# Kernel optimization log

Hardware: AMD Instinct MI355X
Metric: run time of the kernel (lower is better)

Reference implementation:

```python
import jax, jax.numpy as jnp
import numpy as np

B, T, D, H = 4, 2048, 1024, 16
HD = D // H  # head_dim = 64

def setup_inputs() -> dict:
    key = jax.random.key(0)
    k1, k2, k3 = jax.random.split(key, 3)
    s = 1.0 / np.sqrt(D)
    x = jax.random.normal(k1, (B, T, D), dtype=jnp.float32)
    W_qkv = jax.random.normal(k2, (D, 3 * D), dtype=jnp.float32) * s
    W_proj = jax.random.normal(k3, (D, D), dtype=jnp.float32) * s
    return {"x": x, "W_qkv": W_qkv, "W_proj": W_proj}

def reference(x, W_qkv, W_proj):
    Bq, Tq, C = x.shape
    qkv = x @ W_qkv                                   # [B,T,3C]
    q, k, v = jnp.split(qkv, 3, axis=-1)
    def heads(t):  # [B,T,C] -> [B,H,T,HD]
        return t.reshape(Bq, Tq, H, HD).transpose(0, 2, 1, 3)
    q, k, v = heads(q), heads(k), heads(v)
    scale = 1.0 / np.sqrt(HD)
    att = jnp.einsum('bhqd,bhkd->bhqk', q, k) * scale  # [B,H,T,T]
    causal = jnp.tril(jnp.ones((Tq, Tq), dtype=bool))
    att = jnp.where(causal[None, None], att, -jnp.inf)
    att = jax.nn.softmax(att, axis=-1)
    y = jnp.einsum('bhqk,bhkd->bhqd', att, v)          # [B,H,T,HD]
    y = y.transpose(0, 2, 1, 3).reshape(Bq, Tq, C)
    return y @ W_proj
```

## Files before the change

kernel.cpp:

```cpp
#include <hip/hip_runtime.h>

typedef unsigned short ushort_t;
typedef __attribute__((ext_vector_type(8))) __bf16 bf16x8;
typedef __attribute__((ext_vector_type(4))) float f32x4;
typedef __attribute__((ext_vector_type(16))) float f32x16;
typedef __attribute__((ext_vector_type(4))) float float4v;
typedef __attribute__((ext_vector_type(8))) unsigned short ushort8v;
typedef __attribute__((ext_vector_type(4))) unsigned short ushort4v;
typedef __attribute__((ext_vector_type(4))) unsigned uint4v;

#define T_LEN 2048
#define D_DIM 1024
#define NHEAD 16
#define HDIM 64
#define BH 64
#define MROWS 8192
#define PERQKV ((size_t)BH * T_LEN * HDIM)

__device__ __forceinline__ ushort_t f2bf(float f) {
  unsigned u = __builtin_bit_cast(unsigned, f);
  u = (u + 0x7FFFu + ((u >> 16) & 1u)) >> 16;
  return (ushort_t)u;
}

__device__ __forceinline__ float fast_exp2(float x) {
  float r; asm("v_exp_f32 %0, %1" : "=v"(r) : "v"(x)); return r;
}

__device__ __forceinline__ void load_lds16(const ushort_t* g, ushort_t* l) {
  __builtin_amdgcn_global_load_lds((const __attribute__((address_space(1))) void*)g,
                                   (__attribute__((address_space(3))) void*)l, 16, 0, 0);
}

__global__ __launch_bounds__(256) void k_cvt_x(const float* __restrict__ x,
                                               ushort_t* __restrict__ xb) {
  int i = blockIdx.x * 256 + threadIdx.x;
  float4v v = ((const float4v*)x)[i];
  ushort4v o;
  o[0] = f2bf(v[0]); o[1] = f2bf(v[1]); o[2] = f2bf(v[2]); o[3] = f2bf(v[3]);
  ((ushort4v*)xb)[i] = o;
}

__global__ __launch_bounds__(256) void k_transpose(const float* __restrict__ W,
                                                   ushort_t* __restrict__ Wt,
                                                   int R, int C) {
  __shared__ ushort_t tile[32][33];
  int tx = threadIdx.x & 31, ty = threadIdx.x >> 5;
  int r0 = blockIdx.y << 5, c0 = blockIdx.x << 5;
#pragma unroll
  for (int i = 0; i < 4; ++i) {
    int r = ty + i * 8;
    tile[r][tx] = f2bf(W[(size_t)(r0 + r) * C + c0 + tx]);
  }
  __syncthreads();
#pragma unroll
  for (int i = 0; i < 4; ++i) {
    int r = ty + i * 8;
    Wt[(size_t)(c0 + r) * R + r0 + tx] = tile[tx][r];
  }
}

template <int N, int K, int EPI>
__global__ __launch_bounds__(256) void k_gemm(const ushort_t* __restrict__ A,
                                              const ushort_t* __restrict__ Bt,
                                              ushort_t* __restrict__ O16,
                                              float* __restrict__ O32) {
  __shared__ __align__(16) ushort_t Atile[128 * 32];
  __shared__ __align__(16) ushort_t Btile[128 * 32];
  const int tid = threadIdx.x;
  const int lane = tid & 63, w = tid >> 6;
  const int g = lane >> 4, c = lane & 15;
  const int wm = w >> 1, wn = w & 1;
  const int m0 = blockIdx.y * 128, n0 = blockIdx.x * 128;

  f32x4 acc[4][4];
#pragma unroll
  for (int i = 0; i < 4; ++i)
#pragma unroll
    for (int j = 0; j < 4; ++j) acc[i][j] = (f32x4){0.f, 0.f, 0.f, 0.f};

  for (int k0 = 0; k0 < K; k0 += 32) {
    __syncthreads();
#pragma unroll
    for (int r = 0; r < 2; ++r) {
      int flat = r * 256 + tid;
      int row = flat >> 2, slot = flat & 3;
      int gsl = slot ^ (row & 3);
      load_lds16(A + (size_t)(m0 + row) * K + k0 + gsl * 8,
                 &Atile[(r * 256 + w * 64) * 8]);
      load_lds16(Bt + (size_t)(n0 + row) * K + k0 + gsl * 8,
                 &Btile[(r * 256 + w * 64) * 8]);
    }
    __syncthreads();

    bf16x8 af[4], bfr[4];
#pragma unroll
    for (int mi = 0; mi < 4; ++mi) {
      int row = wm * 64 + mi * 16 + c;
      int sl = g ^ (row & 3);
      af[mi] = *(const bf16x8*)&Atile[row * 32 + sl * 8];
    }
#pragma unroll
    for (int ni = 0; ni < 4; ++ni) {
      int row = wn * 64 + ni * 16 + c;
      int sl = g ^ (row & 3);
      bfr[ni] = *(const bf16x8*)&Btile[row * 32 + sl * 8];
    }
#pragma unroll
    for (int mi = 0; mi < 4; ++mi)
#pragma unroll
      for (int ni = 0; ni < 4; ++ni)
        acc[mi][ni] = __builtin_amdgcn_mfma_f32_16x16x32_bf16(af[mi], bfr[ni],
                                                              acc[mi][ni], 0, 0, 0);
  }

#pragma unroll
  for (int mi = 0; mi < 4; ++mi)
#pragma unroll
    for (int ni = 0; ni < 4; ++ni) {
      int n = n0 + wn * 64 + ni * 16 + c;
#pragma unroll
      for (int j = 0; j < 4; ++j) {
        int m = m0 + wm * 64 + mi * 16 + g * 4 + j;
        float v = acc[mi][ni][j];
        if constexpr (EPI == 0) {
          int which = n >> 10, hn = n & 1023;
          int h = hn >> 6, d = hn & 63;
          int b = m >> 11, t = m & 2047;
          if (which == 0) v *= 0.18033688f;
          O16[(size_t)which * PERQKV +
              (((size_t)(b * NHEAD + h) * T_LEN + t) * HDIM + d)] = f2bf(v);
        } else {
          O32[(size_t)m * N + n] = v;
        }
      }
    }
}

template <int NB_TILES, int EPI>
__global__ __launch_bounds__(512, 2) void k_gemm3(const ushort_t* __restrict__ A,
                                                  const ushort_t* __restrict__ Bt,
                                                  ushort_t* __restrict__ O16,
                                                  float* __restrict__ O32) {
  __shared__ __align__(16) ushort_t As[3][128 * 64];
  __shared__ __align__(16) ushort_t Bs[3][256 * 64];
  const int tid = threadIdx.x, lane = tid & 63, w = tid >> 6;
  const int g = lane >> 4, c = lane & 15;
  const int wm = w & 1, wn = w >> 1;
  const int nblk = 64 * NB_TILES;
  const int chunk = nblk >> 3;
  const int bid = blockIdx.x;
  const int logical = (bid & 7) * chunk + (bid >> 3);
  const int mb = logical & 63, nb = logical >> 6;
  const int m0 = mb * 128, n0 = nb * 256;

  const int srow = lane >> 3, sgran = lane & 7;

  auto stage = [&](int t, int buf) {
    const int k0 = t * 64;
#pragma unroll
    for (int l = 0; l < 2; ++l) {
      int r = w * 16 + l * 8 + srow;
      load_lds16(A + (size_t)(m0 + r) * 1024 + k0 + ((sgran ^ (r & 7)) << 3),
                 &As[buf][(w * 16 + l * 8) * 64]);
    }
#pragma unroll
    for (int l = 0; l < 4; ++l) {
      int r = w * 32 + l * 8 + srow;
      load_lds16(Bt + (size_t)(n0 + r) * 1024 + k0 + ((sgran ^ (r & 7)) << 3),
                 &Bs[buf][(w * 32 + l * 8) * 64]);
    }
  };

  f32x4 acc[4][4];
#pragma unroll
  for (int i = 0; i < 4; ++i)
#pragma unroll
    for (int j = 0; j < 4; ++j) acc[i][j] = (f32x4){0.f, 0.f, 0.f, 0.f};

  stage(0, 0);
  stage(1, 1);

  for (int t = 0; t < 16; ++t) {
    if (t < 15) asm volatile("s_waitcnt vmcnt(6)" ::: "memory");
    else        asm volatile("s_waitcnt vmcnt(0)" ::: "memory");
    __builtin_amdgcn_s_barrier();
    __builtin_amdgcn_sched_barrier(0);

    if (t + 2 < 16) stage(t + 2, (t + 2) % 3);

    const int cur = t % 3;
    const ushort_t* abuf = &As[cur][0];
    const ushort_t* bbuf = &Bs[cur][0];
#pragma unroll
    for (int kk = 0; kk < 2; ++kk) {
      bf16x8 af[4], bq[4];
#pragma unroll
      for (int fr = 0; fr < 4; ++fr) {
        int r = wm * 64 + fr * 16 + c;
        af[fr] = *(const bf16x8*)&abuf[r * 64 + (((kk * 4 + g) ^ (r & 7)) << 3)];
      }
#pragma unroll
      for (int fc = 0; fc < 4; ++fc) {
        int r = wn * 64 + fc * 16 + c;
        bq[fc] = *(const bf16x8*)&bbuf[r * 64 + (((kk * 4 + g) ^ (r & 7)) << 3)];
      }
      __builtin_amdgcn_s_setprio(1);
#pragma unroll
      for (int fr = 0; fr < 4; ++fr)
#pragma unroll
        for (int fc = 0; fc < 4; ++fc)
          acc[fr][fc] = __builtin_amdgcn_mfma_f32_16x16x32_bf16(af[fr], bq[fc],
                                                                acc[fr][fc], 0, 0, 0);
      __builtin_amdgcn_s_setprio(0);
    }
  }

#pragma unroll
  for (int fr = 0; fr < 4; ++fr)
#pragma unroll
    for (int fc = 0; fc < 4; ++fc) {
      int n = n0 + wn * 64 + fc * 16 + c;
#pragma unroll
      for (int j = 0; j < 4; ++j) {
        int m = m0 + wm * 64 + fr * 16 + g * 4 + j;
        float v = acc[fr][fc][j];
        if constexpr (EPI == 0) {
          int which = n >> 10, hn = n & 1023;
          int h = hn >> 6, d = hn & 63;
          int b = m >> 11, tt = m & 2047;
          if (which == 0) v *= 0.18033688f;
          O16[(size_t)which * PERQKV +
              (((size_t)(b * NHEAD + h) * T_LEN + tt) * HDIM + d)] = f2bf(v);
        } else {
          O32[(size_t)m * (64 * NB_TILES * 4) + n] = v;
        }
      }
    }
}

__global__ __launch_bounds__(128, 4) void k_attn(const ushort_t* __restrict__ Q,
                                                 const ushort_t* __restrict__ Kv,
                                                 const ushort_t* __restrict__ Vv,
                                                 ushort_t* __restrict__ Y) {
  __shared__ __align__(16) ushort_t Kt[2][64 * 64];
  __shared__ __align__(16) ushort_t Vt[2][64 * 64];

  const int bid = blockIdx.x;
  const int bh = (bid & 7) * 8 + ((bid >> 3) & 7);
  const int pairidx = bid >> 6;
  const int pA = 31 - pairidx, pB = pairidx;
  const int nktA = pA + 1;
  const int total = nktA + pB + 1;

  const int tid = threadIdx.x, lane = tid & 63, w = tid >> 6;
  const int hi = lane >> 5, lc = lane & 31;
  const size_t base = (size_t)bh * (T_LEN * HDIM);

  int q32 = pA * 64 + w * 32;
  bf16x8 qf[4];
#pragma unroll
  for (int st = 0; st < 4; ++st)
    qf[st] = *(const bf16x8*)(Q + base + (size_t)(q32 + lc) * HDIM + st * 16 + hi * 8);

  f32x16 o0, o1;
#pragma unroll
  for (int i = 0; i < 16; ++i) { o0[i] = 0.f; o1[i] = 0.f; }
  float mrun = 0.f, lrun = 0.f;

  const int ksl = tid & 7, krow0 = tid >> 3;
  const int kpair = tid & 31, vk0 = 2 * kpair, vd0 = (tid >> 5) * 8;

  bf16x8 kreg[4];
  ushort8v vreg[4];
  auto stage_issue = [&](int kt) {
    const ushort_t* kb = Kv + base + (size_t)kt * 64 * HDIM;
    const ushort_t* vb = Vv + base + (size_t)kt * 64 * HDIM;
    vreg[0] = *(const ushort8v*)(vb + (size_t)vk0 * HDIM + vd0);
    vreg[1] = *(const ushort8v*)(vb + (size_t)(vk0 + 1) * HDIM + vd0);
    vreg[2] = *(const ushort8v*)(vb + (size_t)vk0 * HDIM + vd0 + 32);
    vreg[3] = *(const ushort8v*)(vb + (size_t)(vk0 + 1) * HDIM + vd0 + 32);
#pragma unroll
    for (int m = 0; m < 4; ++m)
      kreg[m] = *(const bf16x8*)(kb + (size_t)(krow0 + 16 * m) * HDIM + ksl * 8);
  };
  auto stage_write = [&](int buf) {
#pragma unroll
    for (int m = 0; m < 4; ++m) {
      int r = krow0 + 16 * m;
      *(bf16x8*)&Kt[buf][r * 64 + ((ksl ^ (r & 7)) << 3)] = kreg[m];
    }
#pragma unroll
    for (int e = 0; e < 8; ++e) {
      int rd = vd0 + e;
      unsigned pv = (unsigned)vreg[0][e] | ((unsigned)vreg[1][e] << 16);
      *(unsigned*)&Vt[buf][rd * 64 + (((kpair >> 2) ^ (rd & 7)) << 3) + 2 * (kpair & 3)] = pv;
      int rd2 = rd + 32;
      unsigned pv2 = (unsigned)vreg[2][e] | ((unsigned)vreg[3][e] << 16);
      *(unsigned*)&Vt[buf][rd2 * 64 + (((kpair >> 2) ^ (rd2 & 7)) << 3) + 2 * (kpair & 3)] = pv2;
    }
  };

  const int b_ = bh >> 4, h_ = bh & 15;
  auto epilogue = [&]() {
    float lt = lrun + __shfl_xor(lrun, 32);
    float invl = 1.f / lt;
#pragma unroll
    for (int r = 0; r < 16; ++r) {
      int cr = (r & 3) + 8 * (r >> 2) + 4 * hi;
      float iv = __shfl(invl, cr);
      size_t m = (size_t)b_ * T_LEN + q32 + cr;
      Y[m * D_DIM + h_ * HDIM + lc]      = f2bf(o0[r] * iv);
      Y[m * D_DIM + h_ * HDIM + 32 + lc] = f2bf(o1[r] * iv);
    }
  };

  stage_issue(0); stage_write(0);
  stage_issue(1);
  __syncthreads();

  for (int it = 0; it < total; ++it) {
    if (it == nktA) {
      epilogue();
      q32 = pB * 64 + w * 32;
#pragma unroll
      for (int st = 0; st < 4; ++st)
        qf[st] = *(const bf16x8*)(Q + base + (size_t)(q32 + lc) * HDIM + st * 16 + hi * 8);
#pragma unroll
      for (int i = 0; i < 16; ++i) { o0[i] = 0.f; o1[i] = 0.f; }
      mrun = 0.f; lrun = 0.f;
    }
    const int kt = (it < nktA) ? it : it - nktA;
    const int cur = it & 1;
    const ushort_t* kbuf = &Kt[cur][0];
    const ushort_t* vbuf = &Vt[cur][0];

    f32x16 s0, s1;
#pragma unroll
    for (int i = 0; i < 16; ++i) { s0[i] = 0.f; s1[i] = 0.f; }
    __builtin_amdgcn_s_setprio(1);
#pragma unroll
    for (int st = 0; st < 4; ++st) {
      bf16x8 kf0 = *(const bf16x8*)&kbuf[lc * 64 + (((2 * st + hi) ^ (lc & 7)) << 3)];
      s0 = __builtin_amdgcn_mfma_f32_32x32x16_bf16(kf0, qf[st], s0, 0, 0, 0);
    }
#pragma unroll
    for (int st = 0; st < 4; ++st) {
      bf16x8 kf1 = *(const bf16x8*)&kbuf[(32 + lc) * 64 + (((2 * st + hi) ^ (lc & 7)) << 3)];
      s1 = __builtin_amdgcn_mfma_f32_32x32x16_bf16(kf1, qf[st], s1, 0, 0, 0);
    }
    __builtin_amdgcn_s_setprio(0);

    if (kt * 64 + 63 > q32) {
      const int q = q32 + lc;
#pragma unroll
      for (int r = 0; r < 16; ++r) {
        int cr = (r & 3) + 8 * (r >> 2) + 4 * hi;
        if (kt * 64 + cr > q)      s0[r] = -3.0e38f;
        if (kt * 64 + 32 + cr > q) s1[r] = -3.0e38f;
      }
    }

    float tm[8];
#pragma unroll
    for (int i = 0; i < 8; ++i) tm[i] = fmaxf(fmaxf(s0[i], s0[i + 8]), fmaxf(s1[i], s1[i + 8]));
#pragma unroll
    for (int i = 0; i < 4; ++i) tm[i] = fmaxf(tm[i], tm[i + 4]);
    float tmax = fmaxf(fmaxf(tm[0], tm[1]), fmaxf(tm[2], tm[3]));
    tmax = fmaxf(tmax, __shfl_xor(tmax, 32));

    if (!__all(tmax <= mrun + 11.0f)) {
      float mnew = fmaxf(mrun, tmax);
      float sc = fast_exp2(mrun - mnew);
      lrun *= sc; mrun = mnew;
#pragma unroll
      for (int r = 0; r < 16; ++r) {
        int cr = (r & 3) + 8 * (r >> 2) + 4 * hi;
        float scr = __shfl(sc, cr);
        o0[r] *= scr; o1[r] *= scr;
      }
    }

#pragma unroll
    for (int r = 0; r < 16; ++r) s0[r] = fast_exp2(s0[r] - mrun);
#pragma unroll
    for (int r = 0; r < 16; ++r) s1[r] = fast_exp2(s1[r] - mrun);
    {
      float u0 = 0.f, u1 = 0.f, u2 = 0.f, u3 = 0.f;
#pragma unroll
      for (int i = 0; i < 4; ++i) {
        u0 += s0[i];     u1 += s0[i + 4];  u2 += s0[i + 8];  u3 += s0[i + 12];
        u0 += s1[i];     u1 += s1[i + 4];  u2 += s1[i + 8];  u3 += s1[i + 12];
      }
      lrun += (u0 + u1) + (u2 + u3);
    }

    unsigned wv[16];
#pragma unroll
    for (int i = 0; i < 8; ++i) {
      asm("v_cvt_pk_bf16_f32 %0, %1, %2" : "=v"(wv[i])     : "v"(s0[2 * i]), "v"(s0[2 * i + 1]));
      asm("v_cvt_pk_bf16_f32 %0, %1, %2" : "=v"(wv[8 + i]) : "v"(s1[2 * i]), "v"(s1[2 * i + 1]));
    }
    bf16x8 pf[4];
#pragma unroll
    for (int g4 = 0; g4 < 4; ++g4) {
      unsigned a0 = wv[4 * g4], a1 = wv[4 * g4 + 1];
      unsigned a2 = wv[4 * g4 + 2], a3 = wv[4 * g4 + 3];
      asm("v_permlane32_swap_b32 %0, %1" : "+v"(a0), "+v"(a2));
      asm("v_permlane32_swap_b32 %0, %1" : "+v"(a1), "+v"(a3));
      uint4v fw; fw[0] = a0; fw[1] = a1; fw[2] = a2; fw[3] = a3;
      pf[g4] = __builtin_bit_cast(bf16x8, fw);
    }

    __builtin_amdgcn_s_setprio(1);
#pragma unroll
    for (int km = 0; km < 4; ++km) {
      int gsl = ((2 * km + hi) ^ (lc & 7)) << 3;
      bf16x8 vb0 = *(const bf16x8*)&vbuf[lc * 64 + gsl];
      bf16x8 vb1 = *(const bf16x8*)&vbuf[(32 + lc) * 64 + gsl];
      o0 = __builtin_amdgcn_mfma_f32_32x32x16_bf16(pf[km], vb0, o0, 0, 0, 0);
      o1 = __builtin_amdgcn_mfma_f32_32x32x16_bf16(pf[km], vb1, o1, 0, 0, 0);
    }
    __builtin_amdgcn_s_setprio(0);

    if (it + 1 < total) stage_write((it + 1) & 1);
    if (it + 2 < total) {
      int itn = it + 2;
      stage_issue((itn < nktA) ? itn : itn - nktA);
    }
    __syncthreads();
  }

  epilogue();
}

extern "C" void kernel_launch(void* const* d_in, const int* in_sizes, int n_in,
                              void* d_out, int out_size, void* d_ws, size_t ws_size,
                              hipStream_t stream) {
  const float* x     = (const float*)d_in[0];
  const float* Wqkv  = (const float*)d_in[1];
  const float* Wproj = (const float*)d_in[2];
  float* out = (float*)d_out;
  ushort_t* ws = (ushort_t*)d_ws;

  ushort_t* Xb  = ws;
  ushort_t* WqT = Xb  + (size_t)MROWS * D_DIM;
  ushort_t* WpT = WqT + (size_t)3 * D_DIM * D_DIM;
  ushort_t* Qb  = WpT + (size_t)D_DIM * D_DIM;
  ushort_t* Kb  = Qb + PERQKV;
  ushort_t* Vb  = Kb + PERQKV;
  ushort_t* Yb  = Vb + PERQKV;

  k_cvt_x<<<(MROWS * D_DIM / 4) / 256, 256, 0, stream>>>(x, Xb);
  k_transpose<<<dim3(3 * D_DIM / 32, D_DIM / 32), 256, 0, stream>>>(Wqkv, WqT, D_DIM, 3 * D_DIM);
  k_transpose<<<dim3(D_DIM / 32, D_DIM / 32), 256, 0, stream>>>(Wproj, WpT, D_DIM, D_DIM);
  k_gemm<3 * D_DIM, D_DIM, 0><<<dim3(3 * D_DIM / 128, MROWS / 128), 256, 0, stream>>>(Xb, WqT, Qb, nullptr);
  k_attn<<<1024, 128, 0, stream>>>(Qb, Kb, Vb, Yb);
  k_gemm3<4, 1><<<256, 512, 0, stream>>>(Yb, WpT, nullptr, out);
}
```

Baseline: 186.0 us.

## Merge prep kernels, compute softmax denominator via MFMA, use v_perm V staging

New measurement: 175.3 us. 5.8% less time.

```diff
diff --git a/kernel.cpp b/kernel.cpp
--- a/kernel.cpp
+++ b/kernel.cpp
@@ -26,27 +26,39 @@
 __device__ __forceinline__ float fast_exp2(float x) {
   float r; asm("v_exp_f32 %0, %1" : "=v"(r) : "v"(x)); return r;
 }
+__device__ __forceinline__ float fast_rcp(float x) {
+  float r; asm("v_rcp_f32 %0, %1" : "=v"(r) : "v"(x)); return r;
+}
 
 __device__ __forceinline__ void load_lds16(const ushort_t* g, ushort_t* l) {
   __builtin_amdgcn_global_load_lds((const __attribute__((address_space(1))) void*)g,
                                    (__attribute__((address_space(3))) void*)l, 16, 0, 0);
 }
 
-__global__ __launch_bounds__(256) void k_cvt_x(const float* __restrict__ x,
-                                               ushort_t* __restrict__ xb) {
-  int i = blockIdx.x * 256 + threadIdx.x;
-  float4v v = ((const float4v*)x)[i];
-  ushort4v o;
-  o[0] = f2bf(v[0]); o[1] = f2bf(v[1]); o[2] = f2bf(v[2]); o[3] = f2bf(v[3]);
-  ((ushort4v*)xb)[i] = o;
-}
-
-__global__ __launch_bounds__(256) void k_transpose(const float* __restrict__ W,
-                                                   ushort_t* __restrict__ Wt,
-                                                   int R, int C) {
+__global__ __launch_bounds__(256) void k_prep(const float* __restrict__ x,
+                                              const float* __restrict__ Wqkv,
+                                              const float* __restrict__ Wproj,
+                                              ushort_t* __restrict__ xb,
+                                              ushort_t* __restrict__ WqT,
+                                              ushort_t* __restrict__ WpT) {
   __shared__ ushort_t tile[32][33];
-  int tx = threadIdx.x & 31, ty = threadIdx.x >> 5;
-  int r0 = blockIdx.y << 5, c0 = blockIdx.x << 5;
+  int bid = blockIdx.x, tid = threadIdx.x;
+  if (bid < 8192) {
+    int i = bid * 256 + tid;
+    float4v v = ((const float4v*)x)[i];
+    ushort4v o;
+    o[0] = f2bf(v[0]); o[1] = f2bf(v[1]); o[2] = f2bf(v[2]); o[3] = f2bf(v[3]);
+    ((ushort4v*)xb)[i] = o;
+    return;
+  }
+  bid -= 8192;
+  int bx = bid & 127, by = bid >> 7;
+  const float* W; ushort_t* Wt; int C;
+  if (bx < 96) { W = Wqkv; Wt = WqT; C = 3072; }
+  else         { W = Wproj; Wt = WpT; C = 1024; bx -= 96; }
+  const int R = 1024;
+  int tx = tid & 31, ty = tid >> 5;
+  int r0 = by << 5, c0 = bx << 5;
 #pragma unroll
   for (int i = 0; i < 4; ++i) {
     int r = ty + i * 8;
@@ -239,7 +251,7 @@
     }
 }
 
-__global__ __launch_bounds__(128, 4) void k_attn(const ushort_t* __restrict__ Q,
+__global__ __launch_bounds__(128, 2) void k_attn(const ushort_t* __restrict__ Q,
                                                  const ushort_t* __restrict__ Kv,
                                                  const ushort_t* __restrict__ Vv,
                                                  ushort_t* __restrict__ Y) {
@@ -257,16 +269,22 @@
   const int hi = lane >> 5, lc = lane & 31;
   const size_t base = (size_t)bh * (T_LEN * HDIM);
 
+  f32x16 z16;
+#pragma unroll
+  for (int i = 0; i < 16; ++i) z16[i] = 0.f;
+  uint4v ow; ow[0] = ow[1] = ow[2] = ow[3] = 0x3F803F80u;
+  const bf16x8 onesf = __builtin_bit_cast(bf16x8, ow);
+
   int q32 = pA * 64 + w * 32;
   bf16x8 qf[4];
 #pragma unroll
   for (int st = 0; st < 4; ++st)
     qf[st] = *(const bf16x8*)(Q + base + (size_t)(q32 + lc) * HDIM + st * 16 + hi * 8);
 
-  f32x16 o0, o1;
-#pragma unroll
-  for (int i = 0; i < 16; ++i) { o0[i] = 0.f; o1[i] = 0.f; }
-  float mrun = 0.f, lrun = 0.f;
+  f32x16 o0, o1, ol;
+#pragma unroll
+  for (int i = 0; i < 16; ++i) { o0[i] = 0.f; o1[i] = 0.f; ol[i] = 0.f; }
+  float mrun = 0.f;
 
   const int ksl = tid & 7, krow0 = tid >> 3;
   const int kpair = tid & 31, vk0 = 2 * kpair, vd0 = (tid >> 5) * 8;
@@ -290,25 +308,34 @@
       int r = krow0 + 16 * m;
       *(bf16x8*)&Kt[buf][r * 64 + ((ksl ^ (r & 7)) << 3)] = kreg[m];
     }
-#pragma unroll
-    for (int e = 0; e < 8; ++e) {
-      int rd = vd0 + e;
-      unsigned pv = (unsigned)vreg[0][e] | ((unsigned)vreg[1][e] << 16);
-      *(unsigned*)&Vt[buf][rd * 64 + (((kpair >> 2) ^ (rd & 7)) << 3) + 2 * (kpair & 3)] = pv;
+    uint4v a0 = __builtin_bit_cast(uint4v, vreg[0]);
+    uint4v a1 = __builtin_bit_cast(uint4v, vreg[1]);
+    uint4v a2 = __builtin_bit_cast(uint4v, vreg[2]);
+    uint4v a3 = __builtin_bit_cast(uint4v, vreg[3]);
+#pragma unroll
+    for (int i = 0; i < 4; ++i) {
+      unsigned lo, hi2, lo2, hi3;
+      asm("v_perm_b32 %0, %1, %2, %3" : "=v"(lo)  : "v"(a1[i]), "v"(a0[i]), "s"(0x05040100u));
+      asm("v_perm_b32 %0, %1, %2, %3" : "=v"(hi2) : "v"(a1[i]), "v"(a0[i]), "s"(0x07060302u));
+      asm("v_perm_b32 %0, %1, %2, %3" : "=v"(lo2) : "v"(a3[i]), "v"(a2[i]), "s"(0x05040100u));
+      asm("v_perm_b32 %0, %1, %2, %3" : "=v"(hi3) : "v"(a3[i]), "v"(a2[i]), "s"(0x07060302u));
+      int rd = vd0 + 2 * i;
+      *(unsigned*)&Vt[buf][rd * 64 + (((kpair >> 2) ^ (rd & 7)) << 3) + 2 * (kpair & 3)] = lo;
+      int rd1 = rd + 1;
+      *(unsigned*)&Vt[buf][rd1 * 64 + (((kpair >> 2) ^ (rd1 & 7)) << 3) + 2 * (kpair & 3)] = hi2;
       int rd2 = rd + 32;
-      unsigned pv2 = (unsigned)vreg[2][e] | ((unsigned)vreg[3][e] << 16);
-      *(unsigned*)&Vt[buf][rd2 * 64 + (((kpair >> 2) ^ (rd2 & 7)) << 3) + 2 * (kpair & 3)] = pv2;
+      *(unsigned*)&Vt[buf][rd2 * 64 + (((kpair >> 2) ^ (rd2 & 7)) << 3) + 2 * (kpair & 3)] = lo2;
+      int rd3 = rd + 33;
+      *(unsigned*)&Vt[buf][rd3 * 64 + (((kpair >> 2) ^ (rd3 & 7)) << 3) + 2 * (kpair & 3)] = hi3;
     }
   };
 
   const int b_ = bh >> 4, h_ = bh & 15;
   auto epilogue = [&]() {
-    float lt = lrun + __shfl_xor(lrun, 32);
-    float invl = 1.f / lt;
 #pragma unroll
     for (int r = 0; r < 16; ++r) {
       int cr = (r & 3) + 8 * (r >> 2) + 4 * hi;
-      float iv = __shfl(invl, cr);
+      float iv = fast_rcp(ol[r]);
       size_t m = (size_t)b_ * T_LEN + q32 + cr;
       Y[m * D_DIM + h_ * HDIM + lc]      = f2bf(o0[r] * iv);
       Y[m * D_DIM + h_ * HDIM + 32 + lc] = f2bf(o1[r] * iv);
@@ -327,27 +354,28 @@
       for (int st = 0; st < 4; ++st)
         qf[st] = *(const bf16x8*)(Q + base + (size_t)(q32 + lc) * HDIM + st * 16 + hi * 8);
 #pragma unroll
-      for (int i = 0; i < 16; ++i) { o0[i] = 0.f; o1[i] = 0.f; }
-      mrun = 0.f; lrun = 0.f;
+      for (int i = 0; i < 16; ++i) { o0[i] = 0.f; o1[i] = 0.f; ol[i] = 0.f; }
+      mrun = 0.f;
     }
     const int kt = (it < nktA) ? it : it - nktA;
     const int cur = it & 1;
     const ushort_t* kbuf = &Kt[cur][0];
     const ushort_t* vbuf = &Vt[cur][0];
 
-    f32x16 s0, s1;
-#pragma unroll
-    for (int i = 0; i < 16; ++i) { s0[i] = 0.f; s1[i] = 0.f; }
     __builtin_amdgcn_s_setprio(1);
-#pragma unroll
-    for (int st = 0; st < 4; ++st) {
-      bf16x8 kf0 = *(const bf16x8*)&kbuf[lc * 64 + (((2 * st + hi) ^ (lc & 7)) << 3)];
-      s0 = __builtin_amdgcn_mfma_f32_32x32x16_bf16(kf0, qf[st], s0, 0, 0, 0);
-    }
-#pragma unroll
-    for (int st = 0; st < 4; ++st) {
-      bf16x8 kf1 = *(const bf16x8*)&kbuf[(32 + lc) * 64 + (((2 * st + hi) ^ (lc & 7)) << 3)];
-      s1 = __builtin_amdgcn_mfma_f32_32x32x16_bf16(kf1, qf[st], s1, 0, 0, 0);
+    bf16x8 kf0 = *(const bf16x8*)&kbuf[lc * 64 + ((hi ^ (lc & 7)) << 3)];
+    f32x16 s0 = __builtin_amdgcn_mfma_f32_32x32x16_bf16(kf0, qf[0], z16, 0, 0, 0);
+#pragma unroll
+    for (int st = 1; st < 4; ++st) {
+      bf16x8 kf = *(const bf16x8*)&kbuf[lc * 64 + (((2 * st + hi) ^ (lc & 7)) << 3)];
+      s0 = __builtin_amdgcn_mfma_f32_32x32x16_bf16(kf, qf[st], s0, 0, 0, 0);
+    }
+    bf16x8 kg0 = *(const bf16x8*)&kbuf[(32 + lc) * 64 + ((hi ^ (lc & 7)) << 3)];
+    f32x16 s1 = __builtin_amdgcn_mfma_f32_32x32x16_bf16(kg0, qf[0], z16, 0, 0, 0);
+#pragma unroll
+    for (int st = 1; st < 4; ++st) {
+      bf16x8 kg = *(const bf16x8*)&kbuf[(32 + lc) * 64 + (((2 * st + hi) ^ (lc & 7)) << 3)];
+      s1 = __builtin_amdgcn_mfma_f32_32x32x16_bf16(kg, qf[st], s1, 0, 0, 0);
     }
     __builtin_amdgcn_s_setprio(0);
 
@@ -372,12 +400,12 @@
     if (!__all(tmax <= mrun + 11.0f)) {
       float mnew = fmaxf(mrun, tmax);
       float sc = fast_exp2(mrun - mnew);
-      lrun *= sc; mrun = mnew;
+      mrun = mnew;
 #pragma unroll
       for (int r = 0; r < 16; ++r) {
         int cr = (r & 3) + 8 * (r >> 2) + 4 * hi;
         float scr = __shfl(sc, cr);
-        o0[r] *= scr; o1[r] *= scr;
+        o0[r] *= scr; o1[r] *= scr; ol[r] *= scr;
       }
     }
 
@@ -385,15 +413,6 @@
     for (int r = 0; r < 16; ++r) s0[r] = fast_exp2(s0[r] - mrun);
 #pragma unroll
     for (int r = 0; r < 16; ++r) s1[r] = fast_exp2(s1[r] - mrun);
-    {
-      float u0 = 0.f, u1 = 0.f, u2 = 0.f, u3 = 0.f;
-#pragma unroll
-      for (int i = 0; i < 4; ++i) {
-        u0 += s0[i];     u1 += s0[i + 4];  u2 += s0[i + 8];  u3 += s0[i + 12];
-        u0 += s1[i];     u1 += s1[i + 4];  u2 += s1[i + 8];  u3 += s1[i + 12];
-      }
-      lrun += (u0 + u1) + (u2 + u3);
-    }
 
     unsigned wv[16];
 #pragma unroll
@@ -420,6 +439,7 @@
       bf16x8 vb1 = *(const bf16x8*)&vbuf[(32 + lc) * 64 + gsl];
       o0 = __builtin_amdgcn_mfma_f32_32x32x16_bf16(pf[km], vb0, o0, 0, 0, 0);
       o1 = __builtin_amdgcn_mfma_f32_32x32x16_bf16(pf[km], vb1, o1, 0, 0, 0);
+      ol = __builtin_amdgcn_mfma_f32_32x32x16_bf16(pf[km], onesf, ol, 0, 0, 0);
     }
     __builtin_amdgcn_s_setprio(0);
 
@@ -451,9 +471,7 @@
   ushort_t* Vb  = Kb + PERQKV;
   ushort_t* Yb  = Vb + PERQKV;
 
-  k_cvt_x<<<(MROWS * D_DIM / 4) / 256, 256, 0, stream>>>(x, Xb);
-  k_transpose<<<dim3(3 * D_DIM / 32, D_DIM / 32), 256, 0, stream>>>(Wqkv, WqT, D_DIM, 3 * D_DIM);
-  k_transpose<<<dim3(D_DIM / 32, D_DIM / 32), 256, 0, stream>>>(Wproj, WpT, D_DIM, D_DIM);
+  k_prep<<<8192 + 4096, 256, 0, stream>>>(x, Wqkv, Wproj, Xb, WqT, WpT);
   k_gemm<3 * D_DIM, D_DIM, 0><<<dim3(3 * D_DIM / 128, MROWS / 128), 256, 0, stream>>>(Xb, WqT, Qb, nullptr);
   k_attn<<<1024, 128, 0, stream>>>(Qb, Kb, Vb, Yb);
   k_gemm3<4, 1><<<256, 512, 0, stream>>>(Yb, WpT, nullptr, out);
```
